# Kernel tuning notes

Hardware: AMD Instinct MI355X
Metric: run time of the kernel (lower is better)

The kernel has to match this reference:

```python
import jax, jax.numpy as jnp
import numpy as np

D_MODEL = 768
N_HEAD = 12
D_K = D_MODEL // N_HEAD  # 64, also d_v
B, S = 2, 2048


def setup_inputs() -> dict:
    key = jax.random.key(0)
    ks = jax.random.split(key, 8)
    scale = 1.0 / np.sqrt(D_MODEL)
    return {
        "q": jax.random.normal(ks[0], (B, S, D_MODEL), dtype=jnp.float32),
        "k": jax.random.normal(ks[1], (B, S, D_MODEL), dtype=jnp.float32),
        "v": jax.random.normal(ks[2], (B, S, D_MODEL), dtype=jnp.float32),
        "mask": jax.random.randint(ks[3], (B, 1, S, S), 0, 2, dtype=jnp.int32),
        # per-head projection weights, stacked over heads: [H, d_model, d_k]
        "Wq": jax.random.normal(ks[4], (N_HEAD, D_MODEL, D_K), dtype=jnp.float32) * scale,
        "Wk": jax.random.normal(ks[5], (N_HEAD, D_MODEL, D_K), dtype=jnp.float32) * scale,
        "Wv": jax.random.normal(ks[6], (N_HEAD, D_MODEL, D_K), dtype=jnp.float32) * scale,
        # output projection: [n_head*d_v, d_model]
        "Wo": jax.random.normal(ks[7], (N_HEAD * D_K, D_MODEL), dtype=jnp.float32) * scale,
    }


def reference(q, k, v, mask, Wq, Wk, Wv, Wo):
    # Per-head projections (batched over heads instead of a python loop)
    qh = jnp.einsum("bsd,hdk->bhsk", q, Wq)  # [B,H,S,d_k]
    kh = jnp.einsum("bsd,hdk->bhsk", k, Wk)
    vh = jnp.einsum("bsd,hdk->bhsk", v, Wv)
    # Scaled dot-product attention with full score matrix (faithful to source)
    scores = jnp.einsum("bhsk,bhtk->bhst", qh, kh) / jnp.sqrt(jnp.asarray(D_K, qh.dtype))
    scores = jnp.where(mask == 0, jnp.asarray(-1e9, scores.dtype), scores)
    attn = jax.nn.softmax(scores, axis=-1)  # [B,H,S,S]
    out = jnp.einsum("bhst,bhtk->bhsk", attn, vh)  # [B,H,S,d_k]
    # concat heads (matches torch.cat over head outputs along last dim)
    out = out.transpose(0, 2, 1, 3).reshape(out.shape[0], out.shape[2], -1)  # [B,S,H*d_k]
    return out @ Wo  # [B,S,d_model]
```

## Files before the change

### kernel.cpp

```cpp
#include <hip/hip_runtime.h>
#include <stdint.h>

#define S_LEN 2048
#define NH 12
#define DM 768
#define DK 64
#define NB 2
#define MROWS (NB * S_LEN)

typedef __attribute__((ext_vector_type(8))) short short8;
typedef __attribute__((ext_vector_type(4))) float f32x4;
typedef __attribute__((ext_vector_type(4))) uint32_t u32x4;

__device__ __forceinline__ unsigned short bf16rne(float f) {
    union { float f; uint32_t u; } v; v.f = f;
    return (unsigned short)((v.u + 0x7FFFu + ((v.u >> 16) & 1u)) >> 16);
}

__device__ __forceinline__ uint32_t cvtpk(float lo, float hi) {
    uint32_t r;
    asm("v_cvt_pk_bf16_f32 %0, %1, %2" : "=v"(r) : "v"(lo), "v"(hi));
    return r;
}

__global__ __launch_bounds__(256) void prep_kernel(
        const float* __restrict__ Wq, const float* __restrict__ Wk,
        const float* __restrict__ Wv, const float* __restrict__ Wo,
        const int* __restrict__ mask,
        unsigned short* __restrict__ WqT, unsigned short* __restrict__ WkT,
        unsigned short* __restrict__ WvT, unsigned short* __restrict__ WoT,
        uint32_t* __restrict__ pm) {
    int bx = blockIdx.x;
    if (bx < 9216) {
        int which = bx / 2304;
        const float* W = (which == 0) ? Wq : (which == 1) ? Wk : (which == 2) ? Wv : Wo;
        unsigned short* WT = (which == 0) ? WqT : (which == 1) ? WkT : (which == 2) ? WvT : WoT;
        int idx = (bx % 2304) * 256 + threadIdx.x;
        int n = idx / DM, kd = idx % DM;
        float val;
        if (which < 3) { int h = n >> 6, kk = n & 63; val = W[(h * DM + kd) * DK + kk]; }
        else          { val = W[kd * DM + n]; }
        if (which == 0) val *= 0.18033688011112042f;
        WT[idx] = bf16rne(val);
    } else {
        int t = (bx - 9216) * 256 + threadIdx.x;
        const int4* mp = (const int4*)mask;
        int4 a = mp[2 * t], b = mp[2 * t + 1];
        unsigned int by =
            (a.x != 0 ? 1u : 0u)  | (a.y != 0 ? 2u : 0u)  | (a.z != 0 ? 4u : 0u)  | (a.w != 0 ? 8u : 0u) |
            (b.x != 0 ? 16u : 0u) | (b.y != 0 ? 32u : 0u) | (b.z != 0 ? 64u : 0u) | (b.w != 0 ? 128u : 0u);
        ((unsigned char*)pm)[t] = (unsigned char)by;
    }
}

__device__ __forceinline__ void gemm_core_f32A(const float* __restrict__ A,
                                               const unsigned short* __restrict__ BT,
                                               unsigned short* As, unsigned short* Bs,
                                               f32x4 (&acc)[4][4]) {
    const int tid = threadIdx.x;
    const int lane = tid & 63, wid = tid >> 6;
    const int ww = wid & 1, wh = wid >> 1;
    const int quad = lane >> 4, l16 = lane & 15;
    const int lr = lane >> 2;
    const int lc = (lane & 3) * 8;
    typedef __attribute__((address_space(1))) const unsigned int* gp1;
    typedef __attribute__((address_space(3))) unsigned int* lp3;
    const float* Ag0 = A + (size_t)(wid * 32 + lr) * DM + lc;
    const float* Ag1 = A + (size_t)(wid * 32 + 16 + lr) * DM + lc;
    const unsigned short* Bg = BT + (size_t)(wid * 32 + lr) * DM + lc;
    unsigned short* Al = &As[wid * 32 * 32];
    unsigned short* Bl = &Bs[wid * 32 * 32];
    for (int kt = 0; kt < DM; kt += 32) {
        __syncthreads();
        __builtin_amdgcn_global_load_lds((gp1)(const void*)(Bg + kt),            (lp3)(void*)Bl,             16, 0, 0);
        __builtin_amdgcn_global_load_lds((gp1)(const void*)(Bg + 16 * DM + kt),  (lp3)(void*)(Bl + 16 * 32), 16, 0, 0);
        float4 x0 = *(const float4*)(Ag0 + kt), x1 = *(const float4*)(Ag0 + kt + 4);
        float4 y0 = *(const float4*)(Ag1 + kt), y1 = *(const float4*)(Ag1 + kt + 4);
        u32x4 ua, ub;
        ua[0] = cvtpk(x0.x, x0.y); ua[1] = cvtpk(x0.z, x0.w);
        ua[2] = cvtpk(x1.x, x1.y); ua[3] = cvtpk(x1.z, x1.w);
        ub[0] = cvtpk(y0.x, y0.y); ub[1] = cvtpk(y0.z, y0.w);
        ub[2] = cvtpk(y1.x, y1.y); ub[3] = cvtpk(y1.z, y1.w);
        *(u32x4*)&Al[lr * 32 + lc] = ua;
        *(u32x4*)&Al[(16 + lr) * 32 + lc] = ub;
        __syncthreads();
        short8 af[4], bf[4];
#pragma unroll
        for (int i = 0; i < 4; ++i) af[i] = *(const short8*)&As[(wh * 64 + i * 16 + l16) * 32 + quad * 8];
#pragma unroll
        for (int j = 0; j < 4; ++j) bf[j] = *(const short8*)&Bs[(ww * 64 + j * 16 + l16) * 32 + quad * 8];
#pragma unroll
        for (int i = 0; i < 4; ++i)
#pragma unroll
            for (int j = 0; j < 4; ++j)
                acc[i][j] = __builtin_amdgcn_mfma_f32_16x16x32_bf16(af[i], bf[j], acc[i][j], 0, 0, 0);
    }
}

__global__ __launch_bounds__(256) void proj_gemm(
        const float* __restrict__ qf32, const float* __restrict__ kf32,
        const float* __restrict__ vf32,
        const unsigned short* __restrict__ WqT, const unsigned short* __restrict__ WkT,
        const unsigned short* __restrict__ WvT,
        unsigned short* __restrict__ qh, unsigned short* __restrict__ kh,
        unsigned short* __restrict__ vhT) {
    __shared__ __align__(16) unsigned short As[128 * 32];
    __shared__ __align__(16) unsigned short Bs[128 * 32];
    const int bid = blockIdx.x;
    const int xcd = bid & 7, pos = bid >> 3;
    const int widx = xcd * 72 + pos;
    const int oi = widx / 6, by = widx % 6;
    const int z = oi >> 5, bx = oi & 31;
    const float* A = (z == 0) ? qf32 : (z == 1) ? kf32 : vf32;
    const unsigned short* BT = (z == 0) ? WqT : (z == 1) ? WkT : WvT;
    f32x4 acc[4][4] = {};
    gemm_core_f32A(A + (size_t)bx * 128 * DM, BT + (size_t)by * 128 * DM, As, Bs, acc);

    const int tid = threadIdx.x;
    const int lane = tid & 63, wid = tid >> 6;
    const int ww = wid & 1, wh = wid >> 1;
    const int quad = lane >> 4, l16 = lane & 15;
    const int row0 = bx * 128 + wh * 64;
    const int col0 = by * 128 + ww * 64;
    if (z < 2) {
        unsigned short* C = z ? kh : qh;
#pragma unroll
        for (int i = 0; i < 4; ++i)
#pragma unroll
            for (int j = 0; j < 4; ++j)
#pragma unroll
                for (int r = 0; r < 4; ++r)
                    C[(size_t)(row0 + i * 16 + quad * 4 + r) * DM + col0 + j * 16 + l16] = bf16rne(acc[i][j][r]);
    } else {
#pragma unroll
        for (int i = 0; i < 4; ++i)
#pragma unroll
            for (int j = 0; j < 4; ++j) {
                int row = row0 + i * 16 + quad * 4;
                int col = col0 + j * 16 + l16;
                int bb = row >> 11, s = row & 2047;
                int hh = col >> 6, d = col & 63;
                int g = (s >> 2) & 15;
                int pg = (g & 8) | ((g & 3) << 1) | ((g & 4) >> 2);
                int sp = (s & ~63) | (pg << 2) | (s & 3);
                uint32_t lo = (uint32_t)bf16rne(acc[i][j][0]) | ((uint32_t)bf16rne(acc[i][j][1]) << 16);
                uint32_t hi = (uint32_t)bf16rne(acc[i][j][2]) | ((uint32_t)bf16rne(acc[i][j][3]) << 16);
                uint2 o = make_uint2(lo, hi);
                *(uint2*)&vhT[(size_t)((bb * NH + hh) * DK + d) * S_LEN + sp] = o;
            }
    }
}

__global__ __launch_bounds__(256) void attn_kernel(
        const unsigned short* __restrict__ qh, const unsigned short* __restrict__ kh,
        const unsigned short* __restrict__ vhT, const uint32_t* __restrict__ pm,
        unsigned short* __restrict__ pob, float* __restrict__ lsb) {
    const int bid = blockIdx.x;
    const int xcd = bid & 7, pos = bid >> 3;
    const int wkr = xcd * 192 + pos;
    const int qt = wkr & 15;
    const int hz = wkr >> 4;
    const int h = hz % 12;
    const int z = hz / 12;
    const int b = z >> 2, ks = z & 3;
    const int tid = threadIdx.x, w = tid >> 6, lane = tid & 63;
    const int quad = lane >> 4, l16 = lane & 15;
    __shared__ __align__(16) unsigned short SMEM[2 * 2 * 64 * 64];

    const int qrow0 = qt * 128 + w * 32;
    short8 qf[2][2];
#pragma unroll
    for (int mi = 0; mi < 2; ++mi) {
        const size_t qbase = (size_t)(b * S_LEN + qrow0 + mi * 16 + l16) * DM + h * DK;
        qf[mi][0] = *(const short8*)&qh[qbase + quad * 8];
        qf[mi][1] = *(const short8*)&qh[qbase + 32 + quad * 8];
    }
    short8 of = {};
    if (l16 == 0) {
#pragma unroll
        for (int j = 0; j < 8; ++j) of[j] = (short)0x3F80;
    }

    f32x4 out_t[2][4] = {};
    f32x4 outl[2] = {};

    const int srow = tid >> 2, scol = (tid & 3) << 4;
    const int ssw = (srow & 7) << 3;
    const int sc0 = srow * 64 + (scol ^ ssw);
    const int sc1 = srow * 64 + ((scol + 8) ^ ssw);
    const unsigned short* Kg = kh + (size_t)b * S_LEN * DM + h * DK;
    const unsigned short* Vg = vhT + (size_t)((b * NH + h) * DK) * S_LEN;
    const int kt0 = ks * (S_LEN / 4);
    const int NT = (S_LEN / 4) / 64;

    {
        short8 a0 = *(const short8*)&Kg[(size_t)(kt0 + srow) * DM + scol];
        short8 a1 = *(const short8*)&Kg[(size_t)(kt0 + srow) * DM + scol + 8];
        short8 a2 = *(const short8*)&Vg[(size_t)srow * S_LEN + kt0 + scol];
        short8 a3 = *(const short8*)&Vg[(size_t)srow * S_LEN + kt0 + scol + 8];
        *(short8*)&SMEM[sc0] = a0;
        *(short8*)&SMEM[sc1] = a1;
        *(short8*)&SMEM[4096 + sc0] = a2;
        *(short8*)&SMEM[4096 + sc1] = a3;
    }
    __syncthreads();

    int cur = 0;
    for (int t = 0; t < NT; ++t) {
        const int kt = kt0 + t * 64;
        const bool more = (t + 1 < NT);
        short8 kr0, kr1, vr0, vr1;
        if (more) {
            const int kn = kt + 64;
            kr0 = *(const short8*)&Kg[(size_t)(kn + srow) * DM + scol];
            kr1 = *(const short8*)&Kg[(size_t)(kn + srow) * DM + scol + 8];
            vr0 = *(const short8*)&Vg[(size_t)srow * S_LEN + kn + scol];
            vr1 = *(const short8*)&Vg[(size_t)srow * S_LEN + kn + scol + 8];
        }
        uint2 mw[2];
#pragma unroll
        for (int mi = 0; mi < 2; ++mi)
            mw[mi] = *(const uint2*)&pm[(size_t)(b * S_LEN + qrow0 + mi * 16 + l16) * 64 + (kt >> 5)];

        const unsigned short* Ks = SMEM + cur * 8192;
        const unsigned short* Vs = Ks + 4096;

        u32x4 pf32[2][2];
#pragma unroll
        for (int cb = 0; cb < 4; ++cb) {
            const int krw = cb * 16 + l16, ksw = (krw & 7) << 3;
            short8 kf0 = *(const short8*)&Ks[krw * 64 + ((quad * 8) ^ ksw)];
            short8 kf1 = *(const short8*)&Ks[krw * 64 + ((32 + quad * 8) ^ ksw)];
#pragma unroll
            for (int mi = 0; mi < 2; ++mi) {
                f32x4 zz = {0.f, 0.f, 0.f, 0.f};
                zz = __builtin_amdgcn_mfma_f32_16x16x32_bf16(kf0, qf[mi][0], zz, 0, 0, 0);
                zz = __builtin_amdgcn_mfma_f32_16x16x32_bf16(kf1, qf[mi][1], zz, 0, 0, 0);
                uint32_t mword = (cb & 2) ? mw[mi].y : mw[mi].x;
                float e[4];
#pragma unroll
                for (int r = 0; r < 4; ++r) {
                    float ev = __builtin_amdgcn_exp2f(zz[r]);
                    int32_t mneg = __builtin_amdgcn_sbfe((int32_t)mword, ((cb & 1) << 4) + quad * 4 + r, 1);
                    e[r] = __uint_as_float(__float_as_uint(ev) & (uint32_t)mneg);
                }
                pf32[mi][cb >> 1][(cb & 1) * 2 + 0] = cvtpk(e[0], e[1]);
                pf32[mi][cb >> 1][(cb & 1) * 2 + 1] = cvtpk(e[2], e[3]);
            }
        }
        short8 pf[2][2];
#pragma unroll
        for (int mi = 0; mi < 2; ++mi) {
            pf[mi][0] = __builtin_bit_cast(short8, pf32[mi][0]);
            pf[mi][1] = __builtin_bit_cast(short8, pf32[mi][1]);
        }

        __builtin_amdgcn_s_setprio(1);
#pragma unroll
        for (int c2 = 0; c2 < 4; ++c2) {
            const int vrw = c2 * 16 + l16, vsw = (vrw & 7) << 3;
            short8 vf0 = *(const short8*)&Vs[vrw * 64 + ((quad * 8) ^ vsw)];
            short8 vf1 = *(const short8*)&Vs[vrw * 64 + ((32 + quad * 8) ^ vsw)];
#pragma unroll
            for (int mi = 0; mi < 2; ++mi) {
                out_t[mi][c2] = __builtin_amdgcn_mfma_f32_16x16x32_bf16(vf0, pf[mi][0], out_t[mi][c2], 0, 0, 0);
                out_t[mi][c2] = __builtin_amdgcn_mfma_f32_16x16x32_bf16(vf1, pf[mi][1], out_t[mi][c2], 0, 0, 0);
            }
        }
#pragma unroll
        for (int mi = 0; mi < 2; ++mi) {
            outl[mi] = __builtin_amdgcn_mfma_f32_16x16x32_bf16(of, pf[mi][0], outl[mi], 0, 0, 0);
            outl[mi] = __builtin_amdgcn_mfma_f32_16x16x32_bf16(of, pf[mi][1], outl[mi], 0, 0, 0);
        }
        __builtin_amdgcn_s_setprio(0);

        if (more) {
            unsigned short* Kn = SMEM + (cur ^ 1) * 8192;
            *(short8*)&Kn[sc0] = kr0;
            *(short8*)&Kn[sc1] = kr1;
            *(short8*)&Kn[4096 + sc0] = vr0;
            *(short8*)&Kn[4096 + sc1] = vr1;
            __syncthreads();
            cur ^= 1;
        }
    }

    const int pz = z;
    if (quad == 0) {
#pragma unroll
        for (int mi = 0; mi < 2; ++mi)
            lsb[((size_t)pz * NH + h) * S_LEN + qrow0 + mi * 16 + l16] = outl[mi][0];
    }

    __syncthreads();
    unsigned short* Os = SMEM + w * 2048;
#pragma unroll
    for (int mi = 0; mi < 2; ++mi) {
        const int orow = mi * 16 + l16, osw = (orow & 7) << 3;
#pragma unroll
        for (int c2 = 0; c2 < 4; ++c2) {
            uint2 pw2;
            pw2.x = cvtpk(out_t[mi][c2][0], out_t[mi][c2][1]);
            pw2.y = cvtpk(out_t[mi][c2][2], out_t[mi][c2][3]);
            *(uint2*)&Os[orow * 64 + ((c2 * 16 + quad * 4) ^ osw)] = pw2;
        }
    }
    const int ql = lane >> 1, hf = lane & 1;
    const int qsw = (ql & 7) << 3;
    const int qg = qrow0 + ql;
    const size_t orowg = ((size_t)pz * S_LEN + qg) * DM + h * DK + hf * 32;
#pragma unroll
    for (int k2 = 0; k2 < 4; ++k2)
        *(short8*)&pob[orowg + k2 * 8] = *(const short8*)&Os[ql * 64 + ((hf * 32 + k2 * 8) ^ qsw)];
}

__global__ __launch_bounds__(256) void out_gemm(
        const unsigned short* __restrict__ pob, const float* __restrict__ lsb,
        const unsigned short* __restrict__ WoT, float* __restrict__ C) {
    __shared__ __align__(16) unsigned short As[128 * 32];
    __shared__ __align__(16) unsigned short Bs[128 * 32];
    const int bid = blockIdx.x;
    const int xcd = bid & 7, pos = bid >> 3;
    const int widx = xcd * 24 + pos;
    const int bx = widx / 6, by = widx % 6;
    const int tid = threadIdx.x;
    const int lane = tid & 63, wid = tid >> 6;
    const int ww = wid & 1, wh = wid >> 1;
    const int quad = lane >> 4, l16 = lane & 15;
    const int lr = lane >> 2, lc = (lane & 3) * 8;
    typedef __attribute__((address_space(1))) const unsigned int* gp1;
    typedef __attribute__((address_space(3))) unsigned int* lp3;
    const int ra0 = bx * 128 + wid * 32 + lr;
    const int ra1 = ra0 + 16;
    const int bb = bx >> 4;
    const unsigned short* Bg = WoT + (size_t)(by * 128 + wid * 32 + lr) * DM + lc;
    unsigned short* Al = &As[wid * 32 * 32];
    unsigned short* Bl = &Bs[wid * 32 * 32];
    size_t oa0[4], oa1[4];
    int ol0[4], ol1[4];
#pragma unroll
    for (int ksp = 0; ksp < 4; ++ksp) {
        int pz = bb * 4 + ksp;
        oa0[ksp] = ((size_t)pz * S_LEN + (ra0 & 2047)) * DM + lc;
        oa1[ksp] = ((size_t)pz * S_LEN + (ra1 & 2047)) * DM + lc;
        ol0[ksp] = (pz * NH) * S_LEN + (ra0 & 2047);
        ol1[ksp] = (pz * NH) * S_LEN + (ra1 & 2047);
    }
    f32x4 acc[4][4] = {};
    for (int kt = 0; kt < DM; kt += 32) {
        __syncthreads();
        __builtin_amdgcn_global_load_lds((gp1)(const void*)(Bg + kt),           (lp3)(void*)Bl,            16, 0, 0);
        __builtin_amdgcn_global_load_lds((gp1)(const void*)(Bg + 16 * DM + kt), (lp3)(void*)(Bl + 16 * 32), 16, 0, 0);
        const int hh = kt >> 6;
        float l0 = 0.f, l1 = 0.f;
        short8 p0[4], p1[4];
#pragma unroll
        for (int ksp = 0; ksp < 4; ++ksp) {
            p0[ksp] = *(const short8*)&pob[oa0[ksp] + kt];
            p1[ksp] = *(const short8*)&pob[oa1[ksp] + kt];
            l0 += lsb[ol0[ksp] + hh * S_LEN];
            l1 += lsb[ol1[ksp] + hh * S_LEN];
        }
        float rl0 = 1.f / fmaxf(l0, 1e-37f);
        float rl1 = 1.f / fmaxf(l1, 1e-37f);
        u32x4 ua, ub;
#pragma unroll
        for (int e = 0; e < 4; ++e) {
            float f0lo = 0.f, f0hi = 0.f, f1lo = 0.f, f1hi = 0.f;
#pragma unroll
            for (int ksp = 0; ksp < 4; ++ksp) {
                uint32_t w0 = ((const u32x4&)p0[ksp])[e];
                uint32_t w1 = ((const u32x4&)p1[ksp])[e];
                f0lo += __uint_as_float(w0 << 16);
                f0hi += __uint_as_float(w0 & 0xFFFF0000u);
                f1lo += __uint_as_float(w1 << 16);
                f1hi += __uint_as_float(w1 & 0xFFFF0000u);
            }
            ua[e] = cvtpk(f0lo * rl0, f0hi * rl0);
            ub[e] = cvtpk(f1lo * rl1, f1hi * rl1);
        }
        *(u32x4*)&Al[lr * 32 + lc] = ua;
        *(u32x4*)&Al[(16 + lr) * 32 + lc] = ub;
        __syncthreads();
        short8 af[4], bf[4];
#pragma unroll
        for (int i = 0; i < 4; ++i) af[i] = *(const short8*)&As[(wh * 64 + i * 16 + l16) * 32 + quad * 8];
#pragma unroll
        for (int j = 0; j < 4; ++j) bf[j] = *(const short8*)&Bs[(ww * 64 + j * 16 + l16) * 32 + quad * 8];
#pragma unroll
        for (int i = 0; i < 4; ++i)
#pragma unroll
            for (int j = 0; j < 4; ++j)
                acc[i][j] = __builtin_amdgcn_mfma_f32_16x16x32_bf16(af[i], bf[j], acc[i][j], 0, 0, 0);
    }
    const int row0 = bx * 128 + wh * 64;
    const int col0 = by * 128 + ww * 64;
#pragma unroll
    for (int i = 0; i < 4; ++i)
#pragma unroll
        for (int j = 0; j < 4; ++j)
#pragma unroll
            for (int r = 0; r < 4; ++r)
                C[(size_t)(row0 + i * 16 + quad * 4 + r) * DM + col0 + j * 16 + l16] = acc[i][j][r];
}

extern "C" void kernel_launch(void* const* d_in, const int* in_sizes, int n_in,
                              void* d_out, int out_size, void* d_ws, size_t ws_size,
                              hipStream_t stream) {
    const float* q = (const float*)d_in[0];
    const float* k = (const float*)d_in[1];
    const float* v = (const float*)d_in[2];
    const int* mask = (const int*)d_in[3];
    const float* Wq = (const float*)d_in[4];
    const float* Wk = (const float*)d_in[5];
    const float* Wv = (const float*)d_in[6];
    const float* Wo = (const float*)d_in[7];
    float* out = (float*)d_out;

    char* ws = (char*)d_ws;
    size_t off = 0;
    auto alloc = [&](size_t bytes) {
        void* p = ws + off;
        off += (bytes + 255) & ~(size_t)255;
        return p;
    };
    const size_t MAT = (size_t)MROWS * DM * 2;
    const size_t WMAT = (size_t)DM * DM * 2;
    unsigned short* WoT = (unsigned short*)alloc(WMAT);
    unsigned short* qh  = (unsigned short*)alloc(MAT);
    unsigned short* kh  = (unsigned short*)alloc(MAT);
    unsigned short* vhT = (unsigned short*)alloc(MAT);
    uint32_t* pmask     = (uint32_t*)alloc((size_t)NB * S_LEN * 64 * 4);
    float* lsb          = (float*)alloc((size_t)8 * NH * S_LEN * 4);
    unsigned short* WqT = (unsigned short*)alloc(WMAT);
    unsigned short* WkT = (unsigned short*)alloc(WMAT);
    unsigned short* WvT = (unsigned short*)alloc(WMAT);
    unsigned short* pob = WqT;
    (void)alloc((size_t)8 * S_LEN * DM * 2 - 3 * WMAT);

    prep_kernel<<<dim3(9216 + 4096), 256, 0, stream>>>(Wq, Wk, Wv, Wo, mask,
                                                       WqT, WkT, WvT, WoT, pmask);
    proj_gemm<<<dim3(576), 256, 0, stream>>>(q, k, v, WqT, WkT, WvT, qh, kh, vhT);
    attn_kernel<<<dim3(1536), 256, 0, stream>>>(qh, kh, vhT, pmask, pob, lsb);
    out_gemm<<<dim3(192), 256, 0, stream>>>(pob, lsb, WoT, out);
}
```

Measured before the change: 239.7 us.

## Double-buffer projection and output GEMMs; tile-transpose weights through LDS in prep

The projection and output GEMMs now use two LDS buffers and prefetch the next K-slice (A conversion and B global_load_lds) while MFMAs run on the current one. This cuts to one barrier per iteration and hides global load latency. The weight prep kernel now transposes 64x64 tiles through shared memory with vectorised coalesced reads and writes instead of strided per-element gathers. The cost is doubled LDS per block and more live registers, which may lower occupancy.

```diff
diff --git a/kernel.cpp b/kernel.cpp
--- a/kernel.cpp
+++ b/kernel.cpp
@@ -30,70 +30,62 @@
         unsigned short* __restrict__ WqT, unsigned short* __restrict__ WkT,
         unsigned short* __restrict__ WvT, unsigned short* __restrict__ WoT,
         uint32_t* __restrict__ pm) {
-    int bx = blockIdx.x;
-    if (bx < 9216) {
-        int which = bx / 2304;
-        const float* W = (which == 0) ? Wq : (which == 1) ? Wk : (which == 2) ? Wv : Wo;
-        unsigned short* WT = (which == 0) ? WqT : (which == 1) ? WkT : (which == 2) ? WvT : WoT;
-        int idx = (bx % 2304) * 256 + threadIdx.x;
-        int n = idx / DM, kd = idx % DM;
-        float val;
-        if (which < 3) { int h = n >> 6, kk = n & 63; val = W[(h * DM + kd) * DK + kk]; }
-        else          { val = W[kd * DM + n]; }
-        if (which == 0) val *= 0.18033688011112042f;
-        WT[idx] = bf16rne(val);
+    const int bx = blockIdx.x, tid = threadIdx.x;
+    if (bx < 576) {
+        __shared__ __align__(16) unsigned short L[64 * 72];
+        int which, kd0, n0;
+        const float* W;
+        unsigned short* WT;
+        if (bx < 432) {
+            which = bx / 144;
+            int t2 = bx % 144;
+            int h = t2 / 12; kd0 = (t2 % 12) * 64; n0 = h * 64;
+            W = (which == 0) ? Wq : (which == 1) ? Wk : Wv;
+            WT = (which == 0) ? WqT : (which == 1) ? WkT : WvT;
+            const int r = tid >> 2, c0 = (tid & 3) << 4;
+            const size_t roff = ((size_t)(h * 768 + kd0 + r)) * 64 + c0;
+            float4 f[4];
+#pragma unroll
+            for (int i = 0; i < 4; ++i) f[i] = *(const float4*)(W + roff + i * 4);
+            const float scl = (which == 0) ? 0.18033688011112042f : 1.0f;
+#pragma unroll
+            for (int i = 0; i < 4; ++i) {
+                L[(c0 + i * 4 + 0) * 72 + r] = bf16rne(f[i].x * scl);
+                L[(c0 + i * 4 + 1) * 72 + r] = bf16rne(f[i].y * scl);
+                L[(c0 + i * 4 + 2) * 72 + r] = bf16rne(f[i].z * scl);
+                L[(c0 + i * 4 + 3) * 72 + r] = bf16rne(f[i].w * scl);
+            }
+        } else {
+            int t3 = bx - 432;
+            kd0 = (t3 / 12) * 64; n0 = (t3 % 12) * 64;
+            WT = WoT;
+            const int r = tid >> 2, c0 = (tid & 3) << 4;
+            const size_t roff = ((size_t)(kd0 + r)) * 768 + n0 + c0;
+            float4 f[4];
+#pragma unroll
+            for (int i = 0; i < 4; ++i) f[i] = *(const float4*)(Wo + roff + i * 4);
+#pragma unroll
+            for (int i = 0; i < 4; ++i) {
+                L[(c0 + i * 4 + 0) * 72 + r] = bf16rne(f[i].x);
+                L[(c0 + i * 4 + 1) * 72 + r] = bf16rne(f[i].y);
+                L[(c0 + i * 4 + 2) * 72 + r] = bf16rne(f[i].z);
+                L[(c0 + i * 4 + 3) * 72 + r] = bf16rne(f[i].w);
+            }
+        }
+        __syncthreads();
+        const int nl = tid >> 2, cc = (tid & 3) << 4;
+        short8 v0 = *(const short8*)&L[nl * 72 + cc];
+        short8 v1 = *(const short8*)&L[nl * 72 + cc + 8];
+        *(short8*)&WT[(size_t)(n0 + nl) * DM + kd0 + cc] = v0;
+        *(short8*)&WT[(size_t)(n0 + nl) * DM + kd0 + cc + 8] = v1;
     } else {
-        int t = (bx - 9216) * 256 + threadIdx.x;
+        int t = (bx - 576) * 256 + tid;
         const int4* mp = (const int4*)mask;
         int4 a = mp[2 * t], b = mp[2 * t + 1];
         unsigned int by =
             (a.x != 0 ? 1u : 0u)  | (a.y != 0 ? 2u : 0u)  | (a.z != 0 ? 4u : 0u)  | (a.w != 0 ? 8u : 0u) |
             (b.x != 0 ? 16u : 0u) | (b.y != 0 ? 32u : 0u) | (b.z != 0 ? 64u : 0u) | (b.w != 0 ? 128u : 0u);
         ((unsigned char*)pm)[t] = (unsigned char)by;
-    }
-}
-
-__device__ __forceinline__ void gemm_core_f32A(const float* __restrict__ A,
-                                               const unsigned short* __restrict__ BT,
-                                               unsigned short* As, unsigned short* Bs,
-                                               f32x4 (&acc)[4][4]) {
-    const int tid = threadIdx.x;
-    const int lane = tid & 63, wid = tid >> 6;
-    const int ww = wid & 1, wh = wid >> 1;
-    const int quad = lane >> 4, l16 = lane & 15;
-    const int lr = lane >> 2;
-    const int lc = (lane & 3) * 8;
-    typedef __attribute__((address_space(1))) const unsigned int* gp1;
-    typedef __attribute__((address_space(3))) unsigned int* lp3;
-    const float* Ag0 = A + (size_t)(wid * 32 + lr) * DM + lc;
-    const float* Ag1 = A + (size_t)(wid * 32 + 16 + lr) * DM + lc;
-    const unsigned short* Bg = BT + (size_t)(wid * 32 + lr) * DM + lc;
-    unsigned short* Al = &As[wid * 32 * 32];
-    unsigned short* Bl = &Bs[wid * 32 * 32];
-    for (int kt = 0; kt < DM; kt += 32) {
-        __syncthreads();
-        __builtin_amdgcn_global_load_lds((gp1)(const void*)(Bg + kt),            (lp3)(void*)Bl,             16, 0, 0);
-        __builtin_amdgcn_global_load_lds((gp1)(const void*)(Bg + 16 * DM + kt),  (lp3)(void*)(Bl + 16 * 32), 16, 0, 0);
-        float4 x0 = *(const float4*)(Ag0 + kt), x1 = *(const float4*)(Ag0 + kt + 4);
-        float4 y0 = *(const float4*)(Ag1 + kt), y1 = *(const float4*)(Ag1 + kt + 4);
-        u32x4 ua, ub;
-        ua[0] = cvtpk(x0.x, x0.y); ua[1] = cvtpk(x0.z, x0.w);
-        ua[2] = cvtpk(x1.x, x1.y); ua[3] = cvtpk(x1.z, x1.w);
-        ub[0] = cvtpk(y0.x, y0.y); ub[1] = cvtpk(y0.z, y0.w);
-        ub[2] = cvtpk(y1.x, y1.y); ub[3] = cvtpk(y1.z, y1.w);
-        *(u32x4*)&Al[lr * 32 + lc] = ua;
-        *(u32x4*)&Al[(16 + lr) * 32 + lc] = ub;
-        __syncthreads();
-        short8 af[4], bf[4];
-#pragma unroll
-        for (int i = 0; i < 4; ++i) af[i] = *(const short8*)&As[(wh * 64 + i * 16 + l16) * 32 + quad * 8];
-#pragma unroll
-        for (int j = 0; j < 4; ++j) bf[j] = *(const short8*)&Bs[(ww * 64 + j * 16 + l16) * 32 + quad * 8];
-#pragma unroll
-        for (int i = 0; i < 4; ++i)
-#pragma unroll
-            for (int j = 0; j < 4; ++j)
-                acc[i][j] = __builtin_amdgcn_mfma_f32_16x16x32_bf16(af[i], bf[j], acc[i][j], 0, 0, 0);
     }
 }
 
@@ -104,8 +96,8 @@
         const unsigned short* __restrict__ WvT,
         unsigned short* __restrict__ qh, unsigned short* __restrict__ kh,
         unsigned short* __restrict__ vhT) {
-    __shared__ __align__(16) unsigned short As[128 * 32];
-    __shared__ __align__(16) unsigned short Bs[128 * 32];
+    __shared__ __align__(16) unsigned short As[2][128 * 32];
+    __shared__ __align__(16) unsigned short Bs[2][128 * 32];
     const int bid = blockIdx.x;
     const int xcd = bid & 7, pos = bid >> 3;
     const int widx = xcd * 72 + pos;
@@ -113,13 +105,66 @@
     const int z = oi >> 5, bx = oi & 31;
     const float* A = (z == 0) ? qf32 : (z == 1) ? kf32 : vf32;
     const unsigned short* BT = (z == 0) ? WqT : (z == 1) ? WkT : WvT;
-    f32x4 acc[4][4] = {};
-    gemm_core_f32A(A + (size_t)bx * 128 * DM, BT + (size_t)by * 128 * DM, As, Bs, acc);
-
     const int tid = threadIdx.x;
     const int lane = tid & 63, wid = tid >> 6;
     const int ww = wid & 1, wh = wid >> 1;
     const int quad = lane >> 4, l16 = lane & 15;
+    const int lr = lane >> 2, lc = (lane & 3) * 8;
+    typedef __attribute__((address_space(1))) const unsigned int* gp1;
+    typedef __attribute__((address_space(3))) unsigned int* lp3;
+    const float* Ag0 = A + (size_t)(bx * 128 + wid * 32 + lr) * DM + lc;
+    const float* Ag1 = Ag0 + 16 * DM;
+    const unsigned short* Bg = BT + (size_t)(by * 128 + wid * 32 + lr) * DM + lc;
+    const int wb = wid * 1024;
+
+    f32x4 acc[4][4] = {};
+    {
+        float4 x0 = *(const float4*)(Ag0), x1 = *(const float4*)(Ag0 + 4);
+        float4 y0 = *(const float4*)(Ag1), y1 = *(const float4*)(Ag1 + 4);
+        __builtin_amdgcn_global_load_lds((gp1)(const void*)(Bg),           (lp3)(void*)&Bs[0][wb],       16, 0, 0);
+        __builtin_amdgcn_global_load_lds((gp1)(const void*)(Bg + 16 * DM), (lp3)(void*)&Bs[0][wb + 512], 16, 0, 0);
+        u32x4 ua, ub;
+        ua[0] = cvtpk(x0.x, x0.y); ua[1] = cvtpk(x0.z, x0.w);
+        ua[2] = cvtpk(x1.x, x1.y); ua[3] = cvtpk(x1.z, x1.w);
+        ub[0] = cvtpk(y0.x, y0.y); ub[1] = cvtpk(y0.z, y0.w);
+        ub[2] = cvtpk(y1.x, y1.y); ub[3] = cvtpk(y1.z, y1.w);
+        *(u32x4*)&As[0][wb + lr * 32 + lc] = ua;
+        *(u32x4*)&As[0][wb + (16 + lr) * 32 + lc] = ub;
+    }
+    __syncthreads();
+    int cur = 0;
+    for (int kt = 0; kt < DM; kt += 32) {
+        const bool more = (kt + 32) < DM;
+        float4 nx0, nx1, ny0, ny1;
+        if (more) {
+            nx0 = *(const float4*)(Ag0 + kt + 32); nx1 = *(const float4*)(Ag0 + kt + 36);
+            ny0 = *(const float4*)(Ag1 + kt + 32); ny1 = *(const float4*)(Ag1 + kt + 36);
+            __builtin_amdgcn_global_load_lds((gp1)(const void*)(Bg + kt + 32),            (lp3)(void*)&Bs[cur ^ 1][wb],       16, 0, 0);
+            __builtin_amdgcn_global_load_lds((gp1)(const void*)(Bg + kt + 32 + 16 * DM),  (lp3)(void*)&Bs[cur ^ 1][wb + 512], 16, 0, 0);
+        }
+        short8 af[4], bf[4];
+#pragma unroll
+        for (int i = 0; i < 4; ++i) af[i] = *(const short8*)&As[cur][(wh * 64 + i * 16 + l16) * 32 + quad * 8];
+#pragma unroll
+        for (int j = 0; j < 4; ++j) bf[j] = *(const short8*)&Bs[cur][(ww * 64 + j * 16 + l16) * 32 + quad * 8];
+#pragma unroll
+        for (int i = 0; i < 4; ++i)
+#pragma unroll
+            for (int j = 0; j < 4; ++j)
+                acc[i][j] = __builtin_amdgcn_mfma_f32_16x16x32_bf16(af[i], bf[j], acc[i][j], 0, 0, 0);
+        if (more) {
+            u32x4 ua, ub;
+            ua[0] = cvtpk(nx0.x, nx0.y); ua[1] = cvtpk(nx0.z, nx0.w);
+            ua[2] = cvtpk(nx1.x, nx1.y); ua[3] = cvtpk(nx1.z, nx1.w);
+            ub[0] = cvtpk(ny0.x, ny0.y); ub[1] = cvtpk(ny0.z, ny0.w);
+            ub[2] = cvtpk(ny1.x, ny1.y); ub[3] = cvtpk(ny1.z, ny1.w);
+            *(u32x4*)&As[cur ^ 1][wb + lr * 32 + lc] = ua;
+            *(u32x4*)&As[cur ^ 1][wb + (16 + lr) * 32 + lc] = ub;
+        }
+        __syncthreads();
+        cur ^= 1;
+    }
+
     const int row0 = bx * 128 + wh * 64;
     const int col0 = by * 128 + ww * 64;
     if (z < 2) {
@@ -317,8 +362,8 @@
 __global__ __launch_bounds__(256) void out_gemm(
         const unsigned short* __restrict__ pob, const float* __restrict__ lsb,
         const unsigned short* __restrict__ WoT, float* __restrict__ C) {
-    __shared__ __align__(16) unsigned short As[128 * 32];
-    __shared__ __align__(16) unsigned short Bs[128 * 32];
+    __shared__ __align__(16) unsigned short As[2][128 * 32];
+    __shared__ __align__(16) unsigned short Bs[2][128 * 32];
     const int bid = blockIdx.x;
     const int xcd = bid & 7, pos = bid >> 3;
     const int widx = xcd * 24 + pos;
@@ -334,8 +379,7 @@
     const int ra1 = ra0 + 16;
     const int bb = bx >> 4;
     const unsigned short* Bg = WoT + (size_t)(by * 128 + wid * 32 + lr) * DM + lc;
-    unsigned short* Al = &As[wid * 32 * 32];
-    unsigned short* Bl = &Bs[wid * 32 * 32];
+    const int wb = wid * 1024;
     size_t oa0[4], oa1[4];
     int ol0[4], ol1[4];
 #pragma unroll
@@ -347,20 +391,18 @@
         ol1[ksp] = (pz * NH) * S_LEN + (ra1 & 2047);
     }
     f32x4 acc[4][4] = {};
-    for (int kt = 0; kt < DM; kt += 32) {
-        __syncthreads();
-        __builtin_amdgcn_global_load_lds((gp1)(const void*)(Bg + kt),           (lp3)(void*)Bl,            16, 0, 0);
-        __builtin_amdgcn_global_load_lds((gp1)(const void*)(Bg + 16 * DM + kt), (lp3)(void*)(Bl + 16 * 32), 16, 0, 0);
-        const int hh = kt >> 6;
-        float l0 = 0.f, l1 = 0.f;
-        short8 p0[4], p1[4];
-#pragma unroll
-        for (int ksp = 0; ksp < 4; ++ksp) {
-            p0[ksp] = *(const short8*)&pob[oa0[ksp] + kt];
-            p1[ksp] = *(const short8*)&pob[oa1[ksp] + kt];
-            l0 += lsb[ol0[ksp] + hh * S_LEN];
-            l1 += lsb[ol1[ksp] + hh * S_LEN];
-        }
+
+    short8 p0[4], p1[4];
+    float s0[4], s1[4];
+    {
+#pragma unroll
+        for (int ksp = 0; ksp < 4; ++ksp) { s0[ksp] = lsb[ol0[ksp]]; s1[ksp] = lsb[ol1[ksp]]; }
+#pragma unroll
+        for (int ksp = 0; ksp < 4; ++ksp) { p0[ksp] = *(const short8*)&pob[oa0[ksp]]; p1[ksp] = *(const short8*)&pob[oa1[ksp]]; }
+        __builtin_amdgcn_global_load_lds((gp1)(const void*)(Bg),           (lp3)(void*)&Bs[0][wb],       16, 0, 0);
+        __builtin_amdgcn_global_load_lds((gp1)(const void*)(Bg + 16 * DM), (lp3)(void*)&Bs[0][wb + 512], 16, 0, 0);
+        float l0 = s0[0] + s0[1] + s0[2] + s0[3];
+        float l1 = s1[0] + s1[1] + s1[2] + s1[3];
         float rl0 = 1.f / fmaxf(l0, 1e-37f);
         float rl1 = 1.f / fmaxf(l1, 1e-37f);
         u32x4 ua, ub;
@@ -379,19 +421,58 @@
             ua[e] = cvtpk(f0lo * rl0, f0hi * rl0);
             ub[e] = cvtpk(f1lo * rl1, f1hi * rl1);
         }
-        *(u32x4*)&Al[lr * 32 + lc] = ua;
-        *(u32x4*)&Al[(16 + lr) * 32 + lc] = ub;
-        __syncthreads();
+        *(u32x4*)&As[0][wb + lr * 32 + lc] = ua;
+        *(u32x4*)&As[0][wb + (16 + lr) * 32 + lc] = ub;
+    }
+    __syncthreads();
+    int cur = 0;
+    for (int kt = 0; kt < DM; kt += 32) {
+        const bool more = (kt + 32) < DM;
+        if (more) {
+            const int hh = (kt + 32) >> 6;
+#pragma unroll
+            for (int ksp = 0; ksp < 4; ++ksp) { s0[ksp] = lsb[ol0[ksp] + hh * S_LEN]; s1[ksp] = lsb[ol1[ksp] + hh * S_LEN]; }
+#pragma unroll
+            for (int ksp = 0; ksp < 4; ++ksp) { p0[ksp] = *(const short8*)&pob[oa0[ksp] + kt + 32]; p1[ksp] = *(const short8*)&pob[oa1[ksp] + kt + 32]; }
+            __builtin_amdgcn_global_load_lds((gp1)(const void*)(Bg + kt + 32),           (lp3)(void*)&Bs[cur ^ 1][wb],       16, 0, 0);
+            __builtin_amdgcn_global_load_lds((gp1)(const void*)(Bg + kt + 32 + 16 * DM), (lp3)(void*)&Bs[cur ^ 1][wb + 512], 16, 0, 0);
+        }
         short8 af[4], bf[4];
 #pragma unroll
-        for (int i = 0; i < 4; ++i) af[i] = *(const short8*)&As[(wh * 64 + i * 16 + l16) * 32 + quad * 8];
-#pragma unroll
-        for (int j = 0; j < 4; ++j) bf[j] = *(const short8*)&Bs[(ww * 64 + j * 16 + l16) * 32 + quad * 8];
+        for (int i = 0; i < 4; ++i) af[i] = *(const short8*)&As[cur][(wh * 64 + i * 16 + l16) * 32 + quad * 8];
+#pragma unroll
+        for (int j = 0; j < 4; ++j) bf[j] = *(const short8*)&Bs[cur][(ww * 64 + j * 16 + l16) * 32 + quad * 8];
 #pragma unroll
         for (int i = 0; i < 4; ++i)
 #pragma unroll
             for (int j = 0; j < 4; ++j)
                 acc[i][j] = __builtin_amdgcn_mfma_f32_16x16x32_bf16(af[i], bf[j], acc[i][j], 0, 0, 0);
+        if (more) {
+            float l0 = s0[0] + s0[1] + s0[2] + s0[3];
+            float l1 = s1[0] + s1[1] + s1[2] + s1[3];
+            float rl0 = 1.f / fmaxf(l0, 1e-37f);
+            float rl1 = 1.f / fmaxf(l1, 1e-37f);
+            u32x4 ua, ub;
+#pragma unroll
+            for (int e = 0; e < 4; ++e) {
+                float f0lo = 0.f, f0hi = 0.f, f1lo = 0.f, f1hi = 0.f;
+#pragma unroll
+                for (int ksp = 0; ksp < 4; ++ksp) {
+                    uint32_t w0 = ((const u32x4&)p0[ksp])[e];
+                    uint32_t w1 = ((const u32x4&)p1[ksp])[e];
+                    f0lo += __uint_as_float(w0 << 16);
+                    f0hi += __uint_as_float(w0 & 0xFFFF0000u);
+                    f1lo += __uint_as_float(w1 << 16);
+                    f1hi += __uint_as_float(w1 & 0xFFFF0000u);
+                }
+                ua[e] = cvtpk(f0lo * rl0, f0hi * rl0);
+                ub[e] = cvtpk(f1lo * rl1, f1hi * rl1);
+            }
+            *(u32x4*)&As[cur ^ 1][wb + lr * 32 + lc] = ua;
+            *(u32x4*)&As[cur ^ 1][wb + (16 + lr) * 32 + lc] = ub;
+        }
+        __syncthreads();
+        cur ^= 1;
     }
     const int row0 = bx * 128 + wh * 64;
     const int col0 = by * 128 + ww * 64;
@@ -438,8 +519,8 @@
     unsigned short* pob = WqT;
     (void)alloc((size_t)8 * S_LEN * DM * 2 - 3 * WMAT);
 
-    prep_kernel<<<dim3(9216 + 4096), 256, 0, stream>>>(Wq, Wk, Wv, Wo, mask,
-                                                       WqT, WkT, WvT, WoT, pmask);
+    prep_kernel<<<dim3(576 + 4096), 256, 0, stream>>>(Wq, Wk, Wv, Wo, mask,
+                                                      WqT, WkT, WvT, WoT, pmask);
     proj_gemm<<<dim3(576), 256, 0, stream>>>(q, k, v, WqT, WkT, WvT, qh, kh, vhT);
     attn_kernel<<<dim3(1536), 256, 0, stream>>>(qh, kh, vhT, pmask, pob, lsb);
     out_gemm<<<dim3(192), 256, 0, stream>>>(pob, lsb, WoT, out);
```

After: 231.2 us. 1.04x faster.
